# Kernel optimization log

Measured on AMD Instinct MI355X. Metric: run time of the kernel, lower is better.

## Reference

```python
import jax, jax.numpy as jnp
import numpy as np

W_DENSITY, W_COUNT, W_DOMAIN, W_REGIONAL = 100.0, 0.001, 0.5, 1.0
LEVELS = (1, 2, 3)


def setup_inputs() -> dict:
    key = jax.random.key(0)
    k1, k2, k3, k4 = jax.random.split(key, 4)
    B, H, W = 32, 768, 768
    return {
        "pred_density": jax.random.uniform(k1, (B, 1, H, W), dtype=jnp.float32),
        "gt_density": jax.random.uniform(k2, (B, 1, H, W), dtype=jnp.float32),
        "domain_pred_rgb": jax.random.normal(k3, (B, 2), dtype=jnp.float32),
        "domain_pred_thermal": jax.random.normal(k4, (B, 2), dtype=jnp.float32),
    }


def _regional_loss(pred, gt):
    # pred, gt: [B, 1, H, W]; H, W divisible by 2**max(LEVELS)
    B, C, H, W = pred.shape
    total = jnp.float32(0.0)
    last_cells = 1
    for L in LEVELS:
        cells = 2 ** L
        hs, ws = H // cells, W // cells
        # region sums via reshape: [B, C, cells, cells]
        p = pred.reshape(B, C, cells, hs, cells, ws).sum(axis=(3, 5))
        g = gt.reshape(B, C, cells, hs, cells, ws).sum(axis=(3, 5))
        # per-region L1 loss = mean over (B, C), summed over the cells x cells grid
        total = total + jnp.abs(p - g).mean(axis=(0, 1)).sum()
        last_cells = cells
    return total / (len(LEVELS) * last_cells * last_cells)


def _ce_loss(logits, labels):
    # mean over batch of -log_softmax(logits)[label]
    logp = jax.nn.log_softmax(logits, axis=-1)
    return -jnp.take_along_axis(logp, labels[:, None], axis=-1).mean()


def reference(pred_density, gt_density, domain_pred_rgb, domain_pred_thermal):
    B = pred_density.shape[0]
    density_loss = jnp.mean((pred_density - gt_density) ** 2)
    pred_count = pred_density.sum(axis=(2, 3)).squeeze()  # [B]
    gt_count = gt_density.sum(axis=(2, 3)).squeeze()
    count_loss = jnp.abs(pred_count - gt_count).mean()
    regional = _regional_loss(pred_density, gt_density)
    rgb_labels = jnp.zeros((B,), dtype=jnp.int32)
    thermal_labels = jnp.ones((B,), dtype=jnp.int32)
    domain_loss = (_ce_loss(domain_pred_rgb, rgb_labels)
                   + _ce_loss(domain_pred_thermal, thermal_labels)) / 2.0
    total_loss = (W_DENSITY * density_loss + W_COUNT * count_loss
                  + W_REGIONAL * regional + W_DOMAIN * domain_loss)
    return total_loss
```

## Files before the change

kernel.cpp:

```cpp
#include <hip/hip_runtime.h>
#include <math.h>

#define BATCH 32
#define HH 768
#define WW 768
#define NBLK 2048

typedef float v4f __attribute__((ext_vector_type(4)));

__global__ __launch_bounds__(256) void region_reduce(
    const float* __restrict__ pred, const float* __restrict__ gt,
    float* __restrict__ sq_out, float* __restrict__ dws)
{
    const int bid   = blockIdx.x;
    const int b     = bid >> 6;
    const int ri    = (bid >> 3) & 7;
    const int chunk = bid & 7;
    const size_t base = (size_t)b * (HH * WW) + (size_t)(ri * 96 + chunk * 12) * WW;

    const int t = threadIdx.x;
    const int g = t >> 5;
    const int l = t & 31;

    const float* pb = pred + base;
    const float* gb = gt   + base;

    unsigned off[9];
    #pragma unroll
    for (int k = 0; k < 9; ++k) {
        const int q   = l + 32 * k;
        const int row = q / 24;
        const int c   = q - row * 24;
        off[k] = (unsigned)((g * 96 + row * WW + c * 4) * sizeof(float));
    }

    v4f p[9], q4[9];
    #pragma unroll
    for (int k = 0; k < 9; ++k)
        asm volatile("global_load_dwordx4 %0, %1, %2"
                     : "=&v"(p[k]) : "v"(off[k]), "s"(pb));
    #pragma unroll
    for (int k = 0; k < 9; ++k)
        asm volatile("global_load_dwordx4 %0, %1, %2"
                     : "=&v"(q4[k]) : "v"(off[k]), "s"(gb));
    asm volatile("s_waitcnt vmcnt(0)"
                 : "+v"(p[0]), "+v"(p[1]), "+v"(p[2]), "+v"(p[3]), "+v"(p[4]),
                   "+v"(p[5]), "+v"(p[6]), "+v"(p[7]), "+v"(p[8]),
                   "+v"(q4[0]), "+v"(q4[1]), "+v"(q4[2]), "+v"(q4[3]), "+v"(q4[4]),
                   "+v"(q4[5]), "+v"(q4[6]), "+v"(q4[7]), "+v"(q4[8])
                 :: "memory");

    float sq = 0.f, ds = 0.f;
    #pragma unroll
    for (int k = 0; k < 9; ++k) {
        const float dx = p[k][0] - q4[k][0];
        const float dy = p[k][1] - q4[k][1];
        const float dz = p[k][2] - q4[k][2];
        const float dw = p[k][3] - q4[k][3];
        sq += (dx * dx + dy * dy) + (dz * dz + dw * dw);
        ds += (dx + dy) + (dz + dw);
    }

    #pragma unroll
    for (int off_ = 16; off_ > 0; off_ >>= 1) ds += __shfl_down(ds, off_, 64);
    #pragma unroll
    for (int off_ = 32; off_ > 0; off_ >>= 1) sq += __shfl_down(sq, off_, 64);

    if (l == 0) dws[((((b << 3) + ri) << 3) + g) * 8 + chunk] = ds;

    __shared__ float lsq[4];
    const int wave = t >> 6;
    if ((t & 63) == 0) lsq[wave] = sq;
    __syncthreads();
    if (t == 0) sq_out[bid] = (lsq[0] + lsq[1]) + (lsq[2] + lsq[3]);
}

__global__ __launch_bounds__(256) void finalize(
    const float* __restrict__ sq, const float* __restrict__ dws,
    const float* __restrict__ rgb, const float* __restrict__ th,
    float* __restrict__ out)
{
    __shared__ float d[NBLK];
    __shared__ float d2[BATCH * 16];
    __shared__ float d1[BATCH * 4];
    __shared__ float redbuf[4 * 6];
    const int t = threadIdx.x;

    float s_sq = 0.f;
    const float4* sq4 = (const float4*)sq;
    #pragma unroll
    for (int k = 0; k < 2; ++k) {
        const float4 v = sq4[t + 256 * k];
        s_sq += (v.x + v.y) + (v.z + v.w);
    }

    float l3 = 0.f;
    #pragma unroll
    for (int k = 0; k < 8; ++k) {
        const int r = t + 256 * k;
        const float4* dp = (const float4*)(dws + r * 8);
        const float4 a = dp[0], bb = dp[1];
        const float v = ((a.x + a.y) + (a.z + a.w)) + ((bb.x + bb.y) + (bb.z + bb.w));
        d[r] = v;
        l3 += fabsf(v);
    }
    __syncthreads();

    float l2 = 0.f;
    #pragma unroll
    for (int k = 0; k < 2; ++k) {
        const int i = t + 256 * k;
        const int b = i >> 4, r2 = i & 15;
        const int i2 = r2 >> 2, j2 = r2 & 3;
        const float* db = d + b * 64;
        const float v = (db[(2 * i2) * 8 + 2 * j2]     + db[(2 * i2) * 8 + 2 * j2 + 1])
                      + (db[(2 * i2 + 1) * 8 + 2 * j2] + db[(2 * i2 + 1) * 8 + 2 * j2 + 1]);
        d2[i] = v;
        l2 += fabsf(v);
    }
    __syncthreads();

    float l1 = 0.f;
    if (t < BATCH * 4) {
        const int b = t >> 2, r1 = t & 3;
        const int i1 = r1 >> 1, j1 = r1 & 1;
        const float* db = d2 + b * 16;
        const float v = (db[(2 * i1) * 4 + 2 * j1]     + db[(2 * i1) * 4 + 2 * j1 + 1])
                      + (db[(2 * i1 + 1) * 4 + 2 * j1] + db[(2 * i1 + 1) * 4 + 2 * j1 + 1]);
        d1[t] = v;
        l1 = fabsf(v);
    }
    __syncthreads();

    float cnt = 0.f, dom = 0.f;
    if (t < BATCH) {
        const float c = (d1[t * 4] + d1[t * 4 + 1]) + (d1[t * 4 + 2] + d1[t * 4 + 3]);
        cnt = fabsf(c);
        const float x0 = rgb[t * 2], x1 = rgb[t * 2 + 1];
        const float mx = fmaxf(x0, x1);
        dom  = (mx + logf(expf(x0 - mx) + expf(x1 - mx))) - x0;
        const float y0 = th[t * 2], y1 = th[t * 2 + 1];
        const float my = fmaxf(y0, y1);
        dom += (my + logf(expf(y0 - my) + expf(y1 - my))) - y1;
    }

    float vals[6] = {s_sq, l3, l2, l1, cnt, dom};
    #pragma unroll
    for (int off = 32; off > 0; off >>= 1) {
        #pragma unroll
        for (int j = 0; j < 6; ++j) vals[j] += __shfl_down(vals[j], off, 64);
    }
    const int wave = t >> 6;
    if ((t & 63) == 0) {
        #pragma unroll
        for (int j = 0; j < 6; ++j) redbuf[wave * 6 + j] = vals[j];
    }
    __syncthreads();
    if (t == 0) {
        float S[6];
        #pragma unroll
        for (int j = 0; j < 6; ++j)
            S[j] = (redbuf[j] + redbuf[6 + j]) + (redbuf[12 + j] + redbuf[18 + j]);
        const float density  = S[0] / (float)((size_t)BATCH * HH * WW);
        const float count_l  = S[4] / (float)BATCH;
        const float regional = ((S[3] + S[2] + S[1]) / (float)BATCH) / 192.0f;
        const float domain   = S[5] / 64.0f;
        out[0] = 100.0f * density + 0.001f * count_l + 1.0f * regional + 0.5f * domain;
    }
}

extern "C" void kernel_launch(void* const* d_in, const int* in_sizes, int n_in,
                              void* d_out, int out_size, void* d_ws, size_t ws_size,
                              hipStream_t stream) {
    const float* pred = (const float*)d_in[0];
    const float* gt   = (const float*)d_in[1];
    const float* rgb  = (const float*)d_in[2];
    const float* th   = (const float*)d_in[3];
    float* out = (float*)d_out;

    float* sq  = (float*)d_ws;
    float* dws = sq + NBLK;

    region_reduce<<<NBLK, 256, 0, stream>>>(pred, gt, sq, dws);
    finalize<<<1, 256, 0, stream>>>(sq, dws, rgb, th, out);
}
```

Baseline: 170.4 us.

## Process four row chunks per block with double-buffered software-pipelined loads

```diff
diff --git a/kernel.cpp b/kernel.cpp
--- a/kernel.cpp
+++ b/kernel.cpp
@@ -4,7 +4,9 @@
 #define BATCH 32
 #define HH 768
 #define WW 768
-#define NBLK 2048
+#define NBLK 512
+#define NREG 2048
+#define CHUNK_FLOATS (12 * WW)
 
 typedef float v4f __attribute__((ext_vector_type(4)));
 
@@ -12,11 +14,11 @@
     const float* __restrict__ pred, const float* __restrict__ gt,
     float* __restrict__ sq_out, float* __restrict__ dws)
 {
-    const int bid   = blockIdx.x;
-    const int b     = bid >> 6;
-    const int ri    = (bid >> 3) & 7;
-    const int chunk = bid & 7;
-    const size_t base = (size_t)b * (HH * WW) + (size_t)(ri * 96 + chunk * 12) * WW;
+    const int bid  = blockIdx.x;
+    const int b    = bid >> 4;
+    const int ri   = (bid >> 1) & 7;
+    const int half = bid & 1;
+    const size_t base = (size_t)b * (HH * WW) + (size_t)(ri * 96 + half * 48) * WW;
 
     const int t = threadIdx.x;
     const int g = t >> 5;
@@ -34,39 +36,78 @@
         off[k] = (unsigned)((g * 96 + row * WW + c * 4) * sizeof(float));
     }
 
-    v4f p[9], q4[9];
-    #pragma unroll
-    for (int k = 0; k < 9; ++k)
-        asm volatile("global_load_dwordx4 %0, %1, %2"
-                     : "=&v"(p[k]) : "v"(off[k]), "s"(pb));
-    #pragma unroll
-    for (int k = 0; k < 9; ++k)
-        asm volatile("global_load_dwordx4 %0, %1, %2"
-                     : "=&v"(q4[k]) : "v"(off[k]), "s"(gb));
-    asm volatile("s_waitcnt vmcnt(0)"
-                 : "+v"(p[0]), "+v"(p[1]), "+v"(p[2]), "+v"(p[3]), "+v"(p[4]),
-                   "+v"(p[5]), "+v"(p[6]), "+v"(p[7]), "+v"(p[8]),
-                   "+v"(q4[0]), "+v"(q4[1]), "+v"(q4[2]), "+v"(q4[3]), "+v"(q4[4]),
-                   "+v"(q4[5]), "+v"(q4[6]), "+v"(q4[7]), "+v"(q4[8])
-                 :: "memory");
-
-    float sq = 0.f, ds = 0.f;
-    #pragma unroll
-    for (int k = 0; k < 9; ++k) {
-        const float dx = p[k][0] - q4[k][0];
-        const float dy = p[k][1] - q4[k][1];
-        const float dz = p[k][2] - q4[k][2];
-        const float dw = p[k][3] - q4[k][3];
-        sq += (dx * dx + dy * dy) + (dz * dz + dw * dw);
-        ds += (dx + dy) + (dz + dw);
-    }
-
-    #pragma unroll
-    for (int off_ = 16; off_ > 0; off_ >>= 1) ds += __shfl_down(ds, off_, 64);
+    v4f pA[9], qA[9], pB[9], qB[9];
+    float sq = 0.f, ds0, ds1, ds2, ds3;
+
+#define ISSUE(P, Q, PP, GG)                                                   \
+    do {                                                                      \
+        _Pragma("unroll")                                                     \
+        for (int k = 0; k < 9; ++k)                                           \
+            asm volatile("global_load_dwordx4 %0, %1, %2"                     \
+                         : "=&v"((P)[k]) : "v"(off[k]), "s"(PP));             \
+        _Pragma("unroll")                                                     \
+        for (int k = 0; k < 9; ++k)                                           \
+            asm volatile("global_load_dwordx4 %0, %1, %2"                     \
+                         : "=&v"((Q)[k]) : "v"(off[k]), "s"(GG));             \
+    } while (0)
+
+#define TIE18(P, Q, N)                                                        \
+    asm volatile("s_waitcnt vmcnt(" N ")"                                     \
+                 : "+v"((P)[0]), "+v"((P)[1]), "+v"((P)[2]), "+v"((P)[3]),    \
+                   "+v"((P)[4]), "+v"((P)[5]), "+v"((P)[6]), "+v"((P)[7]),    \
+                   "+v"((P)[8]),                                              \
+                   "+v"((Q)[0]), "+v"((Q)[1]), "+v"((Q)[2]), "+v"((Q)[3]),    \
+                   "+v"((Q)[4]), "+v"((Q)[5]), "+v"((Q)[6]), "+v"((Q)[7]),    \
+                   "+v"((Q)[8])                                               \
+                 :: "memory")
+
+#define CONSUME(P, Q, DS)                                                     \
+    do {                                                                      \
+        float lds_ = 0.f, lsq_ = 0.f;                                         \
+        _Pragma("unroll")                                                     \
+        for (int k = 0; k < 9; ++k) {                                         \
+            const float dx = (P)[k][0] - (Q)[k][0];                           \
+            const float dy = (P)[k][1] - (Q)[k][1];                           \
+            const float dz = (P)[k][2] - (Q)[k][2];                           \
+            const float dw = (P)[k][3] - (Q)[k][3];                           \
+            lsq_ += (dx * dx + dy * dy) + (dz * dz + dw * dw);                \
+            lds_ += (dx + dy) + (dz + dw);                                    \
+        }                                                                     \
+        sq += lsq_;                                                           \
+        (DS) = lds_;                                                          \
+    } while (0)
+
+    ISSUE(pA, qA, pb, gb);
+    ISSUE(pB, qB, pb + CHUNK_FLOATS, gb + CHUNK_FLOATS);
+    TIE18(pA, qA, "18");
+    CONSUME(pA, qA, ds0);
+    ISSUE(pA, qA, pb + 2 * CHUNK_FLOATS, gb + 2 * CHUNK_FLOATS);
+    TIE18(pB, qB, "18");
+    CONSUME(pB, qB, ds1);
+    ISSUE(pB, qB, pb + 3 * CHUNK_FLOATS, gb + 3 * CHUNK_FLOATS);
+    TIE18(pA, qA, "18");
+    CONSUME(pA, qA, ds2);
+    TIE18(pB, qB, "0");
+    CONSUME(pB, qB, ds3);
+
+#undef ISSUE
+#undef TIE18
+#undef CONSUME
+
+    #pragma unroll
+    for (int off_ = 16; off_ > 0; off_ >>= 1) {
+        ds0 += __shfl_down(ds0, off_, 64);
+        ds1 += __shfl_down(ds1, off_, 64);
+        ds2 += __shfl_down(ds2, off_, 64);
+        ds3 += __shfl_down(ds3, off_, 64);
+    }
     #pragma unroll
     for (int off_ = 32; off_ > 0; off_ >>= 1) sq += __shfl_down(sq, off_, 64);
 
-    if (l == 0) dws[((((b << 3) + ri) << 3) + g) * 8 + chunk] = ds;
+    if (l == 0) {
+        float4* dp = (float4*)(dws + (((((b << 3) + ri) << 3) + g) << 3) + (half << 2));
+        *dp = make_float4(ds0, ds1, ds2, ds3);
+    }
 
     __shared__ float lsq[4];
     const int wave = t >> 6;
@@ -80,18 +121,16 @@
     const float* __restrict__ rgb, const float* __restrict__ th,
     float* __restrict__ out)
 {
-    __shared__ float d[NBLK];
+    __shared__ float d[NREG];
     __shared__ float d2[BATCH * 16];
     __shared__ float d1[BATCH * 4];
     __shared__ float redbuf[4 * 6];
     const int t = threadIdx.x;
 
     float s_sq = 0.f;
-    const float4* sq4 = (const float4*)sq;
-    #pragma unroll
-    for (int k = 0; k < 2; ++k) {
-        const float4 v = sq4[t + 256 * k];
-        s_sq += (v.x + v.y) + (v.z + v.w);
+    if (t < NBLK / 4) {
+        const float4 v = ((const float4*)sq)[t];
+        s_sq = (v.x + v.y) + (v.z + v.w);
     }
 
     float l3 = 0.f;
```

Result: slower. 174.0 us (+2.1%).
